# Kernel tuning notes

Hardware: AMD Instinct MI355X
Metric: run time of the kernel (lower is better)

Reference implementation:

```python
import jax, jax.numpy as jnp
import numpy as np

NUM_EXPERTS = 8
HIDDEN = 2048
INTER = 4096
TOKENS = 1024


def setup_inputs() -> dict:
    key = jax.random.key(0)
    k1, k2, k3, k4 = jax.random.split(key, 4)
    hidden_states = jax.random.normal(k1, (TOKENS, HIDDEN), dtype=jnp.float32)
    router_logits = jax.random.normal(k2, (TOKENS, NUM_EXPERTS), dtype=jnp.float32)
    # W13: fused [gate_proj; up_proj] per expert: [E, 2*I, H]
    W13 = jax.random.normal(k3, (NUM_EXPERTS, 2 * INTER, HIDDEN), dtype=jnp.float32) * (1.0 / np.sqrt(HIDDEN))
    # W2: down_proj per expert: [E, H, I]
    W2 = jax.random.normal(k4, (NUM_EXPERTS, HIDDEN, INTER), dtype=jnp.float32) * (1.0 / np.sqrt(INTER))
    return {"hidden_states": hidden_states, "router_logits": router_logits,
            "W13": W13, "W2": W2, "top_k": 2}


def reference(hidden_states, router_logits, W13, W2, top_k):
    # Mixtral-style MoE: softmax -> top_k -> renormalize -> SwiGLU experts -> weighted combine
    T, E = router_logits.shape
    probs = jax.nn.softmax(router_logits.astype(jnp.float32), axis=-1)
    topk_w, topk_idx = jax.lax.top_k(probs, top_k)          # [T, k]
    topk_w = topk_w / jnp.sum(topk_w, axis=-1, keepdims=True)  # renormalize=True
    # dense routing matrix [T, E] with zeros for unselected experts
    routing = jnp.zeros((T, E), dtype=hidden_states.dtype)
    routing = routing.at[jnp.arange(T)[:, None], topk_idx].add(topk_w.astype(hidden_states.dtype))
    # grouped gate_up GEMM: [T, E, 2I]
    gate_up = jnp.einsum('th,eoh->teo', hidden_states, W13)
    gate, up = jnp.split(gate_up, 2, axis=-1)               # each [T, E, I]
    act = jax.nn.silu(gate) * up                            # SwiGLU
    # grouped down GEMM: [T, E, H]
    expert_out = jnp.einsum('tei,ehi->teh', act, W2)
    # scatter-combine with routing weights
    return jnp.einsum('teh,te->th', expert_out, routing)
```

## Files before the change

### kernel.cpp

```cpp
#include <hip/hip_runtime.h>

#define NEXP 8
#define HID 2048
#define INTER 4096
#define NTOK 1024
#define CAP 512
#define BK 64

#define FENCE() do { asm volatile("" ::: "memory"); __builtin_amdgcn_sched_barrier(0); } while (0)

typedef short bf8 __attribute__((ext_vector_type(8)));
typedef float f4  __attribute__((ext_vector_type(4)));

__device__ __forceinline__ unsigned short f2bf(float f) {
  unsigned u = __builtin_bit_cast(unsigned, f);
  u += 0x7fffu + ((u >> 16) & 1u);
  return (unsigned short)(u >> 16);
}

__device__ __forceinline__ void ld_lds16(const void* g, void* l) {
  __builtin_amdgcn_global_load_lds(
      (const __attribute__((address_space(1))) unsigned*)g,
      (__attribute__((address_space(3))) unsigned*)l, 16, 0, 0);
}

__device__ __forceinline__ void packB8(unsigned short* dst, float4 a, float4 b) {
  union { bf8 v; unsigned short u[8]; } p;
  p.u[0] = f2bf(a.x); p.u[1] = f2bf(a.y); p.u[2] = f2bf(a.z); p.u[3] = f2bf(a.w);
  p.u[4] = f2bf(b.x); p.u[5] = f2bf(b.y); p.u[6] = f2bf(b.z); p.u[7] = f2bf(b.w);
  *(bf8*)dst = p.v;
}

__global__ void k_router(const float* __restrict__ lg, int* __restrict__ cnt,
                         int* __restrict__ tok, float* __restrict__ wgt) {
  __shared__ int lc[NEXP];
  int t = threadIdx.x;
  if (t < NEXP) lc[t] = 0;
  __syncthreads();
  float l[NEXP];
#pragma unroll
  for (int i = 0; i < NEXP; ++i) l[i] = lg[t * NEXP + i];
  int i1 = 0; float v1 = l[0];
#pragma unroll
  for (int i = 1; i < NEXP; ++i) if (l[i] > v1) { v1 = l[i]; i1 = i; }
  int i2 = -1; float v2 = -3.4e38f;
#pragma unroll
  for (int i = 0; i < NEXP; ++i) if (i != i1 && l[i] > v2) { v2 = l[i]; i2 = i; }
  float e2 = __expf(v2 - v1);
  float w1 = 1.f / (1.f + e2);
  float w2 = e2 / (1.f + e2);
  int s1 = atomicAdd(&lc[i1], 1);
  if (s1 < CAP) { tok[i1 * CAP + s1] = t; wgt[i1 * CAP + s1] = w1; }
  int s2 = atomicAdd(&lc[i2], 1);
  if (s2 < CAP) { tok[i2 * CAP + s2] = t; wgt[i2 * CAP + s2] = w2; }
  __syncthreads();
  if (t < NEXP) cnt[t] = lc[t];
}

__global__ void k_gather(const float* __restrict__ hid, const int* __restrict__ cnt,
                         const int* __restrict__ tok, unsigned short* __restrict__ hs) {
  int b = blockIdx.x;
  int e = b >> 9, s = b & (CAP - 1);
  if (s >= cnt[e]) return;
  int t = tok[e * CAP + s];
  const float4* src = (const float4*)(hid + (size_t)t * HID);
  ushort4* dst = (ushort4*)(hs + ((size_t)e * CAP + s) * HID);
  for (int i = threadIdx.x; i < HID / 4; i += 128) {
    float4 v = src[i];
    ushort4 o = make_ushort4(f2bf(v.x), f2bf(v.y), f2bf(v.z), f2bf(v.w));
    dst[i] = o;
  }
}

__global__ __launch_bounds__(256, 2) void k_gemm1(
    const unsigned short* __restrict__ hs, const float* __restrict__ W13,
    const int* __restrict__ cnt, unsigned short* __restrict__ act) {
  int e = blockIdx.x >> 7;
  int n0 = (blockIdx.x & 127) * 32;
  int count = cnt[e];
  if (count <= 0) return;
  if (count > CAP) count = CAP;

  __shared__ __align__(16) unsigned short lA[3 * 128 * BK];
  __shared__ __align__(16) unsigned short lB[2][64 * BK];

  int tid = threadIdx.x;
  int wv = tid >> 6, ln = tid & 63;
  int quad = ln >> 4, l16 = ln & 15;

  const unsigned short* A0 = hs + (size_t)e * CAP * HID;
  const float* B = W13 + (size_t)e * (2 * INTER) * HID;

  int r0 = tid >> 3;
  int bc = tid & 7;
  const float* g0 = B + (size_t)(n0 + r0) * HID + bc * 8;
  const float* g1 = B + (size_t)(INTER + n0 + r0) * HID + bc * 8;
  int wpo0 = r0 * BK + ((bc ^ (r0 & 7)) * 8);
  int wpo1 = (r0 + 32) * BK + ((bc ^ (r0 & 7)) * 8);

  for (int m0 = 0; m0 < count; m0 += 384) {
    int rem = count - m0;
    int mtLive = (rem + 127) >> 7; if (mtLive > 3) mtLive = 3;
    int nIss = mtLive * 4;
    const unsigned short* A = A0 + (size_t)m0 * HID;

    f4 acc[3][2][2][2];
#pragma unroll
    for (int a = 0; a < 3; ++a)
#pragma unroll
      for (int b2 = 0; b2 < 2; ++b2)
#pragma unroll
        for (int c = 0; c < 2; ++c)
#pragma unroll
          for (int d = 0; d < 2; ++d) acc[a][b2][c][d] = (f4){0.f, 0.f, 0.f, 0.f};

    float4 c0 = *(const float4*)(g0 + 0);
    float4 c1 = *(const float4*)(g0 + 4);
    float4 c2 = *(const float4*)(g1 + 0);
    float4 c3 = *(const float4*)(g1 + 4);
    FENCE();
    for (int j = 0; j < nIss; ++j) {
      int rl = j * 32 + (tid >> 3);
      int cg = (tid & 7) ^ (rl & 7);
      ld_lds16(A + (size_t)rl * HID + cg * 8, &lA[j * 2048 + wv * 512]);
    }
    FENCE();
    packB8(&lB[0][wpo0], c0, c1);
    packB8(&lB[0][wpo1], c2, c3);
    c0 = *(const float4*)(g0 + BK);
    c1 = *(const float4*)(g0 + BK + 4);
    c2 = *(const float4*)(g1 + BK);
    c3 = *(const float4*)(g1 + BK + 4);
    FENCE();
    asm volatile("s_waitcnt vmcnt(4) lgkmcnt(0)" ::: "memory");
    __builtin_amdgcn_sched_barrier(0);
    __builtin_amdgcn_s_barrier();
    FENCE();

    int kb = 0;
    for (int k0 = 0; k0 < HID; k0 += BK, kb ^= 1) {
      const unsigned short* lBk = lB[kb];
      __builtin_amdgcn_s_setprio(1);
#pragma unroll
      for (int ks = 0; ks < 2; ++ks) {
        int c = ks * 4 + quad;
        bf8 bg[2][2];
#pragma unroll
        for (int mat = 0; mat < 2; ++mat)
#pragma unroll
          for (int ns = 0; ns < 2; ++ns) {
            int br = mat * 32 + ns * 16 + l16;
            bg[mat][ns] = *(const bf8*)&lBk[br * BK + ((c ^ (br & 7)) * 8)];
          }
#pragma unroll
        for (int mt = 0; mt < 3; ++mt) {
          if (mt >= mtLive) break;
#pragma unroll
          for (int ms = 0; ms < 2; ++ms) {
            int rl = mt * 128 + wv * 32 + ms * 16 + l16;
            bf8 a = *(const bf8*)&lA[rl * BK + ((c ^ (rl & 7)) * 8)];
#pragma unroll
            for (int mat = 0; mat < 2; ++mat)
#pragma unroll
              for (int ns = 0; ns < 2; ++ns)
                acc[mt][ms][mat][ns] = __builtin_amdgcn_mfma_f32_16x16x32_bf16(
                    a, bg[mat][ns], acc[mt][ms][mat][ns], 0, 0, 0);
          }
        }
      }
      __builtin_amdgcn_s_setprio(0);
      FENCE();
      __builtin_amdgcn_s_barrier();
      FENCE();
      if (k0 + BK < HID) {
        packB8(&lB[kb ^ 1][wpo0], c0, c1);
        packB8(&lB[kb ^ 1][wpo1], c2, c3);
        for (int j = 0; j < nIss; ++j) {
          int rl = j * 32 + (tid >> 3);
          int cg = (tid & 7) ^ (rl & 7);
          ld_lds16(A + (size_t)rl * HID + (k0 + BK) + cg * 8, &lA[j * 2048 + wv * 512]);
        }
        FENCE();
        int kn = (k0 + 2 * BK < HID) ? (k0 + 2 * BK) : 0;
        c0 = *(const float4*)(g0 + kn);
        c1 = *(const float4*)(g0 + kn + 4);
        c2 = *(const float4*)(g1 + kn);
        c3 = *(const float4*)(g1 + kn + 4);
        FENCE();
        asm volatile("s_waitcnt vmcnt(4) lgkmcnt(0)" ::: "memory");
        __builtin_amdgcn_sched_barrier(0);
        __builtin_amdgcn_s_barrier();
        FENCE();
      }
    }

    size_t actE = (size_t)e * CAP * INTER;
#pragma unroll
    for (int mt = 0; mt < 3; ++mt) {
      if (mt >= mtLive) break;
#pragma unroll
      for (int ms = 0; ms < 2; ++ms) {
        int rbase = m0 + mt * 128 + wv * 32 + ms * 16 + quad * 4;
#pragma unroll
        for (int ns = 0; ns < 2; ++ns) {
          int col = n0 + ns * 16 + l16;
#pragma unroll
          for (int r = 0; r < 4; ++r) {
            int row = rbase + r;
            if (row < count) {
              float g = acc[mt][ms][0][ns][r];
              float u = acc[mt][ms][1][ns][r];
              float sv = g / (1.f + __expf(-g)) * u;
              act[actE + (size_t)row * INTER + col] = f2bf(sv);
            }
          }
        }
      }
    }
  }
}

__global__ __launch_bounds__(256, 2) void k_gemm2(
    const unsigned short* __restrict__ act, const float* __restrict__ W2,
    const int* __restrict__ cnt, const int* __restrict__ tok,
    const float* __restrict__ wgt, float* __restrict__ out) {
  int e = blockIdx.x >> 6;
  int n0 = (blockIdx.x & 63) * 32;
  int count = cnt[e];
  if (count <= 0) return;
  if (count > CAP) count = CAP;

  __shared__ __align__(16) unsigned short lA[3 * 128 * BK];
  __shared__ __align__(16) unsigned short lB[2][32 * BK];

  int tid = threadIdx.x;
  int wv = tid >> 6, ln = tid & 63;
  int quad = ln >> 4, l16 = ln & 15;

  const unsigned short* A0 = act + (size_t)e * CAP * INTER;
  const float* B = W2 + (size_t)e * HID * INTER;

  int r0 = tid >> 3;
  int bc = tid & 7;
  const float* g0 = B + (size_t)(n0 + r0) * INTER + bc * 8;
  int wpo0 = r0 * BK + ((bc ^ (r0 & 7)) * 8);

  for (int m0 = 0; m0 < count; m0 += 384) {
    int rem = count - m0;
    int mtLive = (rem + 127) >> 7; if (mtLive > 3) mtLive = 3;
    int nIss = mtLive * 4;
    const unsigned short* A = A0 + (size_t)m0 * INTER;

    f4 acc[3][2][2];
#pragma unroll
    for (int a = 0; a < 3; ++a)
#pragma unroll
      for (int b2 = 0; b2 < 2; ++b2)
#pragma unroll
        for (int c = 0; c < 2; ++c) acc[a][b2][c] = (f4){0.f, 0.f, 0.f, 0.f};

    float4 c0 = *(const float4*)(g0 + 0);
    float4 c1 = *(const float4*)(g0 + 4);
    FENCE();
    for (int j = 0; j < nIss; ++j) {
      int rl = j * 32 + (tid >> 3);
      int cg = (tid & 7) ^ (rl & 7);
      ld_lds16(A + (size_t)rl * INTER + cg * 8, &lA[j * 2048 + wv * 512]);
    }
    FENCE();
    packB8(&lB[0][wpo0], c0, c1);
    c0 = *(const float4*)(g0 + BK);
    c1 = *(const float4*)(g0 + BK + 4);
    FENCE();
    asm volatile("s_waitcnt vmcnt(2) lgkmcnt(0)" ::: "memory");
    __builtin_amdgcn_sched_barrier(0);
    __builtin_amdgcn_s_barrier();
    FENCE();

    int kb = 0;
    for (int k0 = 0; k0 < INTER; k0 += BK, kb ^= 1) {
      const unsigned short* lBk = lB[kb];
      __builtin_amdgcn_s_setprio(1);
#pragma unroll
      for (int ks = 0; ks < 2; ++ks) {
        int c = ks * 4 + quad;
        bf8 bb[2];
#pragma unroll
        for (int ns = 0; ns < 2; ++ns) {
          int br = ns * 16 + l16;
          bb[ns] = *(const bf8*)&lBk[br * BK + ((c ^ (br & 7)) * 8)];
        }
#pragma unroll
        for (int mt = 0; mt < 3; ++mt) {
          if (mt >= mtLive) break;
#pragma unroll
          for (int ms = 0; ms < 2; ++ms) {
            int rl = mt * 128 + wv * 32 + ms * 16 + l16;
            bf8 a = *(const bf8*)&lA[rl * BK + ((c ^ (rl & 7)) * 8)];
#pragma unroll
            for (int ns = 0; ns < 2; ++ns)
              acc[mt][ms][ns] = __builtin_amdgcn_mfma_f32_16x16x32_bf16(
                  a, bb[ns], acc[mt][ms][ns], 0, 0, 0);
          }
        }
      }
      __builtin_amdgcn_s_setprio(0);
      FENCE();
      __builtin_amdgcn_s_barrier();
      FENCE();
      if (k0 + BK < INTER) {
        packB8(&lB[kb ^ 1][wpo0], c0, c1);
        for (int j = 0; j < nIss; ++j) {
          int rl = j * 32 + (tid >> 3);
          int cg = (tid & 7) ^ (rl & 7);
          ld_lds16(A + (size_t)rl * INTER + (k0 + BK) + cg * 8, &lA[j * 2048 + wv * 512]);
        }
        FENCE();
        int kn = (k0 + 2 * BK < INTER) ? (k0 + 2 * BK) : 0;
        c0 = *(const float4*)(g0 + kn);
        c1 = *(const float4*)(g0 + kn + 4);
        FENCE();
        asm volatile("s_waitcnt vmcnt(2) lgkmcnt(0)" ::: "memory");
        __builtin_amdgcn_sched_barrier(0);
        __builtin_amdgcn_s_barrier();
        FENCE();
      }
    }

#pragma unroll
    for (int mt = 0; mt < 3; ++mt) {
      if (mt >= mtLive) break;
#pragma unroll
      for (int ms = 0; ms < 2; ++ms) {
        int rbase = m0 + mt * 128 + wv * 32 + ms * 16 + quad * 4;
#pragma unroll
        for (int ns = 0; ns < 2; ++ns) {
          int col = n0 + ns * 16 + l16;
#pragma unroll
          for (int r = 0; r < 4; ++r) {
            int row = rbase + r;
            if (row < count) {
              int t = tok[e * CAP + row];
              float w = wgt[e * CAP + row];
              atomicAdd(out + (size_t)t * HID + col, w * acc[mt][ms][ns][r]);
            }
          }
        }
      }
    }
  }
}

extern "C" void kernel_launch(void* const* d_in, const int* in_sizes, int n_in,
                              void* d_out, int out_size, void* d_ws, size_t ws_size,
                              hipStream_t stream) {
  const float* hidden = (const float*)d_in[0];
  const float* logits = (const float*)d_in[1];
  const float* W13    = (const float*)d_in[2];
  const float* W2     = (const float*)d_in[3];
  float* out = (float*)d_out;

  char* wsb = (char*)d_ws;
  int*   cnt = (int*)wsb;
  int*   tok = (int*)(wsb + 256);
  float* wgt = (float*)(wsb + 256 + NEXP * CAP * 4);
  unsigned short* hs  = (unsigned short*)(wsb + 256 + NEXP * CAP * 8);
  unsigned short* actb = hs + (size_t)NEXP * CAP * HID;

  hipMemsetAsync(d_out, 0, (size_t)out_size * sizeof(float), stream);
  k_router<<<1, 1024, 0, stream>>>(logits, cnt, tok, wgt);
  k_gather<<<NEXP * CAP, 128, 0, stream>>>(hidden, cnt, tok, hs);
  k_gemm1<<<NEXP * 128, 256, 0, stream>>>(hs, W13, cnt, actb);
  k_gemm2<<<NEXP * 64, 256, 0, stream>>>(actb, W2, cnt, tok, wgt, out);
}
```

Measured before the change: 988.6 us.

## Double-buffer A tiles in LDS and issue next-K loads before MFMA compute

Both expert GEMM kernels now keep two LDS buffers for the A (activation) tile. The loads for the next K slice of A and B are issued before the MFMA work on the current slice, which removes one barrier per K step and overlaps the global-to-LDS copies with compute. To fit two A buffers in LDS, the M tile per pass shrinks from 384 to 256 rows. Experts with more than 256 tokens therefore take two passes, and B is only prefetched one step ahead with a full vmcnt(0) wait. The LDS footprint also grows, which may limit residency at 2 blocks per CU.

```diff
diff --git a/kernel.cpp b/kernel.cpp
--- a/kernel.cpp
+++ b/kernel.cpp
@@ -81,7 +81,7 @@
   if (count <= 0) return;
   if (count > CAP) count = CAP;
 
-  __shared__ __align__(16) unsigned short lA[3 * 128 * BK];
+  __shared__ __align__(16) unsigned short lA[2][256 * BK];
   __shared__ __align__(16) unsigned short lB[2][64 * BK];
 
   int tid = threadIdx.x;
@@ -98,15 +98,15 @@
   int wpo0 = r0 * BK + ((bc ^ (r0 & 7)) * 8);
   int wpo1 = (r0 + 32) * BK + ((bc ^ (r0 & 7)) * 8);
 
-  for (int m0 = 0; m0 < count; m0 += 384) {
+  for (int m0 = 0; m0 < count; m0 += 256) {
     int rem = count - m0;
-    int mtLive = (rem + 127) >> 7; if (mtLive > 3) mtLive = 3;
+    int mtLive = (rem + 127) >> 7; if (mtLive > 2) mtLive = 2;
     int nIss = mtLive * 4;
     const unsigned short* A = A0 + (size_t)m0 * HID;
 
-    f4 acc[3][2][2][2];
-#pragma unroll
-    for (int a = 0; a < 3; ++a)
+    f4 acc[2][2][2][2];
+#pragma unroll
+    for (int a = 0; a < 2; ++a)
 #pragma unroll
       for (int b2 = 0; b2 < 2; ++b2)
 #pragma unroll
@@ -114,32 +114,46 @@
 #pragma unroll
           for (int d = 0; d < 2; ++d) acc[a][b2][c][d] = (f4){0.f, 0.f, 0.f, 0.f};
 
+    __syncthreads();
+
+    for (int j = 0; j < nIss; ++j) {
+      int rl = j * 32 + (tid >> 3);
+      int cg = (tid & 7) ^ (rl & 7);
+      ld_lds16(A + (size_t)rl * HID + cg * 8, &lA[0][j * 2048 + wv * 512]);
+    }
+    FENCE();
     float4 c0 = *(const float4*)(g0 + 0);
     float4 c1 = *(const float4*)(g0 + 4);
     float4 c2 = *(const float4*)(g1 + 0);
     float4 c3 = *(const float4*)(g1 + 4);
     FENCE();
-    for (int j = 0; j < nIss; ++j) {
-      int rl = j * 32 + (tid >> 3);
-      int cg = (tid & 7) ^ (rl & 7);
-      ld_lds16(A + (size_t)rl * HID + cg * 8, &lA[j * 2048 + wv * 512]);
-    }
-    FENCE();
+    asm volatile("s_waitcnt vmcnt(0)" ::: "memory");
     packB8(&lB[0][wpo0], c0, c1);
     packB8(&lB[0][wpo1], c2, c3);
-    c0 = *(const float4*)(g0 + BK);
-    c1 = *(const float4*)(g0 + BK + 4);
-    c2 = *(const float4*)(g1 + BK);
-    c3 = *(const float4*)(g1 + BK + 4);
-    FENCE();
-    asm volatile("s_waitcnt vmcnt(4) lgkmcnt(0)" ::: "memory");
+    FENCE();
+    asm volatile("s_waitcnt lgkmcnt(0)" ::: "memory");
     __builtin_amdgcn_sched_barrier(0);
     __builtin_amdgcn_s_barrier();
     FENCE();
 
-    int kb = 0;
-    for (int k0 = 0; k0 < HID; k0 += BK, kb ^= 1) {
-      const unsigned short* lBk = lB[kb];
+    int cur = 0;
+    for (int k0 = 0; k0 < HID; k0 += BK, cur ^= 1) {
+      int nxt = k0 + BK;
+      if (nxt < HID) {
+        for (int j = 0; j < nIss; ++j) {
+          int rl = j * 32 + (tid >> 3);
+          int cg = (tid & 7) ^ (rl & 7);
+          ld_lds16(A + (size_t)rl * HID + nxt + cg * 8, &lA[cur ^ 1][j * 2048 + wv * 512]);
+        }
+        FENCE();
+        c0 = *(const float4*)(g0 + nxt);
+        c1 = *(const float4*)(g0 + nxt + 4);
+        c2 = *(const float4*)(g1 + nxt);
+        c3 = *(const float4*)(g1 + nxt + 4);
+        FENCE();
+      }
+      const unsigned short* lBk = lB[cur];
+      const unsigned short* lAk = lA[cur];
       __builtin_amdgcn_s_setprio(1);
 #pragma unroll
       for (int ks = 0; ks < 2; ++ks) {
@@ -153,12 +167,12 @@
             bg[mat][ns] = *(const bf8*)&lBk[br * BK + ((c ^ (br & 7)) * 8)];
           }
 #pragma unroll
-        for (int mt = 0; mt < 3; ++mt) {
+        for (int mt = 0; mt < 2; ++mt) {
           if (mt >= mtLive) break;
 #pragma unroll
           for (int ms = 0; ms < 2; ++ms) {
             int rl = mt * 128 + wv * 32 + ms * 16 + l16;
-            bf8 a = *(const bf8*)&lA[rl * BK + ((c ^ (rl & 7)) * 8)];
+            bf8 a = *(const bf8*)&lAk[rl * BK + ((c ^ (rl & 7)) * 8)];
 #pragma unroll
             for (int mat = 0; mat < 2; ++mat)
 #pragma unroll
@@ -170,24 +184,12 @@
       }
       __builtin_amdgcn_s_setprio(0);
       FENCE();
-      __builtin_amdgcn_s_barrier();
-      FENCE();
-      if (k0 + BK < HID) {
-        packB8(&lB[kb ^ 1][wpo0], c0, c1);
-        packB8(&lB[kb ^ 1][wpo1], c2, c3);
-        for (int j = 0; j < nIss; ++j) {
-          int rl = j * 32 + (tid >> 3);
-          int cg = (tid & 7) ^ (rl & 7);
-          ld_lds16(A + (size_t)rl * HID + (k0 + BK) + cg * 8, &lA[j * 2048 + wv * 512]);
-        }
-        FENCE();
-        int kn = (k0 + 2 * BK < HID) ? (k0 + 2 * BK) : 0;
-        c0 = *(const float4*)(g0 + kn);
-        c1 = *(const float4*)(g0 + kn + 4);
-        c2 = *(const float4*)(g1 + kn);
-        c3 = *(const float4*)(g1 + kn + 4);
-        FENCE();
-        asm volatile("s_waitcnt vmcnt(4) lgkmcnt(0)" ::: "memory");
+      if (nxt < HID) {
+        asm volatile("s_waitcnt vmcnt(0)" ::: "memory");
+        packB8(&lB[cur ^ 1][wpo0], c0, c1);
+        packB8(&lB[cur ^ 1][wpo1], c2, c3);
+        FENCE();
+        asm volatile("s_waitcnt lgkmcnt(0)" ::: "memory");
         __builtin_amdgcn_sched_barrier(0);
         __builtin_amdgcn_s_barrier();
         FENCE();
@@ -196,7 +198,7 @@
 
     size_t actE = (size_t)e * CAP * INTER;
 #pragma unroll
-    for (int mt = 0; mt < 3; ++mt) {
+    for (int mt = 0; mt < 2; ++mt) {
       if (mt >= mtLive) break;
 #pragma unroll
       for (int ms = 0; ms < 2; ++ms) {
@@ -230,7 +232,7 @@
   if (count <= 0) return;
   if (count > CAP) count = CAP;
 
-  __shared__ __align__(16) unsigned short lA[3 * 128 * BK];
+  __shared__ __align__(16) unsigned short lA[2][256 * BK];
   __shared__ __align__(16) unsigned short lB[2][32 * BK];
 
   int tid = threadIdx.x;
@@ -245,41 +247,55 @@
   const float* g0 = B + (size_t)(n0 + r0) * INTER + bc * 8;
   int wpo0 = r0 * BK + ((bc ^ (r0 & 7)) * 8);
 
-  for (int m0 = 0; m0 < count; m0 += 384) {
+  for (int m0 = 0; m0 < count; m0 += 256) {
     int rem = count - m0;
-    int mtLive = (rem + 127) >> 7; if (mtLive > 3) mtLive = 3;
+    int mtLive = (rem + 127) >> 7; if (mtLive > 2) mtLive = 2;
     int nIss = mtLive * 4;
     const unsigned short* A = A0 + (size_t)m0 * INTER;
 
-    f4 acc[3][2][2];
-#pragma unroll
-    for (int a = 0; a < 3; ++a)
+    f4 acc[2][2][2];
+#pragma unroll
+    for (int a = 0; a < 2; ++a)
 #pragma unroll
       for (int b2 = 0; b2 < 2; ++b2)
 #pragma unroll
         for (int c = 0; c < 2; ++c) acc[a][b2][c] = (f4){0.f, 0.f, 0.f, 0.f};
 
-    float4 c0 = *(const float4*)(g0 + 0);
-    float4 c1 = *(const float4*)(g0 + 4);
-    FENCE();
+    __syncthreads();
+
     for (int j = 0; j < nIss; ++j) {
       int rl = j * 32 + (tid >> 3);
       int cg = (tid & 7) ^ (rl & 7);
-      ld_lds16(A + (size_t)rl * INTER + cg * 8, &lA[j * 2048 + wv * 512]);
-    }
-    FENCE();
+      ld_lds16(A + (size_t)rl * INTER + cg * 8, &lA[0][j * 2048 + wv * 512]);
+    }
+    FENCE();
+    float4 c0 = *(const float4*)(g0 + 0);
+    float4 c1 = *(const float4*)(g0 + 4);
+    FENCE();
+    asm volatile("s_waitcnt vmcnt(0)" ::: "memory");
     packB8(&lB[0][wpo0], c0, c1);
-    c0 = *(const float4*)(g0 + BK);
-    c1 = *(const float4*)(g0 + BK + 4);
-    FENCE();
-    asm volatile("s_waitcnt vmcnt(2) lgkmcnt(0)" ::: "memory");
+    FENCE();
+    asm volatile("s_waitcnt lgkmcnt(0)" ::: "memory");
     __builtin_amdgcn_sched_barrier(0);
     __builtin_amdgcn_s_barrier();
     FENCE();
 
-    int kb = 0;
-    for (int k0 = 0; k0 < INTER; k0 += BK, kb ^= 1) {
-      const unsigned short* lBk = lB[kb];
+    int cur = 0;
+    for (int k0 = 0; k0 < INTER; k0 += BK, cur ^= 1) {
+      int nxt = k0 + BK;
+      if (nxt < INTER) {
+        for (int j = 0; j < nIss; ++j) {
+          int rl = j * 32 + (tid >> 3);
+          int cg = (tid & 7) ^ (rl & 7);
+          ld_lds16(A + (size_t)rl * INTER + nxt + cg * 8, &lA[cur ^ 1][j * 2048 + wv * 512]);
+        }
+        FENCE();
+        c0 = *(const float4*)(g0 + nxt);
+        c1 = *(const float4*)(g0 + nxt + 4);
+        FENCE();
+      }
+      const unsigned short* lBk = lB[cur];
+      const unsigned short* lAk = lA[cur];
       __builtin_amdgcn_s_setprio(1);
 #pragma unroll
       for (int ks = 0; ks < 2; ++ks) {
@@ -291,12 +307,12 @@
           bb[ns] = *(const bf8*)&lBk[br * BK + ((c ^ (br & 7)) * 8)];
         }
 #pragma unroll
-        for (int mt = 0; mt < 3; ++mt) {
+        for (int mt = 0; mt < 2; ++mt) {
           if (mt >= mtLive) break;
 #pragma unroll
           for (int ms = 0; ms < 2; ++ms) {
             int rl = mt * 128 + wv * 32 + ms * 16 + l16;
-            bf8 a = *(const bf8*)&lA[rl * BK + ((c ^ (rl & 7)) * 8)];
+            bf8 a = *(const bf8*)&lAk[rl * BK + ((c ^ (rl & 7)) * 8)];
 #pragma unroll
             for (int ns = 0; ns < 2; ++ns)
               acc[mt][ms][ns] = __builtin_amdgcn_mfma_f32_16x16x32_bf16(
@@ -306,21 +322,11 @@
       }
       __builtin_amdgcn_s_setprio(0);
       FENCE();
-      __builtin_amdgcn_s_barrier();
-      FENCE();
-      if (k0 + BK < INTER) {
-        packB8(&lB[kb ^ 1][wpo0], c0, c1);
-        for (int j = 0; j < nIss; ++j) {
-          int rl = j * 32 + (tid >> 3);
-          int cg = (tid & 7) ^ (rl & 7);
-          ld_lds16(A + (size_t)rl * INTER + (k0 + BK) + cg * 8, &lA[j * 2048 + wv * 512]);
-        }
-        FENCE();
-        int kn = (k0 + 2 * BK < INTER) ? (k0 + 2 * BK) : 0;
-        c0 = *(const float4*)(g0 + kn);
-        c1 = *(const float4*)(g0 + kn + 4);
-        FENCE();
-        asm volatile("s_waitcnt vmcnt(2) lgkmcnt(0)" ::: "memory");
+      if (nxt < INTER) {
+        asm volatile("s_waitcnt vmcnt(0)" ::: "memory");
+        packB8(&lB[cur ^ 1][wpo0], c0, c1);
+        FENCE();
+        asm volatile("s_waitcnt lgkmcnt(0)" ::: "memory");
         __builtin_amdgcn_sched_barrier(0);
         __builtin_amdgcn_s_barrier();
         FENCE();
@@ -328,7 +334,7 @@
     }
 
 #pragma unroll
-    for (int mt = 0; mt < 3; ++mt) {
+    for (int mt = 0; mt < 2; ++mt) {
       if (mt >= mtLive) break;
 #pragma unroll
       for (int ms = 0; ms < 2; ++ms) {
```

Result: slower. 1.093 ms (+10.6%).
